# Kernel optimization log

Measured on AMD Instinct MI355X. Metric: run time of the kernel, lower is better.

The kernel has to match this reference:

```python
import jax, jax.numpy as jnp
import numpy as np

NH = 16  # num_heads


def _ln(x, eps=1e-6):
    m = x.mean(-1, keepdims=True)
    v = ((x - m) ** 2).mean(-1, keepdims=True)
    return (x - m) * jax.lax.rsqrt(v + eps)


def _mod(z, sh, sc):
    return z * (1 + sc[:, None, :]) + sh[:, None, :]


def _attn(q, k, v, out_w, out_b, nh=NH):
    B, S, E = q.shape
    hd = E // nh
    q = q.reshape(B, S, nh, hd)
    k = k.reshape(B, -1, nh, hd)
    v = v.reshape(B, -1, nh, hd)
    s = jnp.einsum('bqhd,bkhd->bhqk', q, k) / float(np.sqrt(hd))
    a = jax.nn.softmax(s, axis=-1)
    o = jnp.einsum('bhqk,bkhd->bqhd', a, v).reshape(B, S, E)
    return o @ out_w.T + out_b


def setup_inputs() -> dict:
    key = jax.random.key(0)
    ks = jax.random.split(key, 40)
    E, L, Ne, I, p, C, clip, Kd = 1024, 2, 8, 4096, 2, 4, 768, 1536
    N = (64 // p) ** 2
    n = lambda k, shape, s=0.02: (jax.random.normal(k, shape, jnp.float32) * s)
    inp = {
        'x': jax.random.normal(ks[0], (2, C, 64, 64), jnp.float32),
        't': jax.random.uniform(ks[1], (2,), jnp.float32) * 1000.0,
        'clip_vec': jax.random.normal(ks[2], (2, clip), jnp.float32),
        'qwen_context': jax.random.normal(ks[3], (2, 256, Kd), jnp.float32),
        'conv_w': n(ks[4], (E, C, p, p)),
        'conv_b': n(ks[5], (E,)),
        'pos_embed': n(ks[6], (1, N, E)),
        'tmlp_w1': n(ks[7], (256, 256)), 'tmlp_b1': n(ks[8], (256,)),
        'tmlp_w2': n(ks[9], (256, 256)), 'tmlp_b2': n(ks[10], (256,)),
        'cond_w': n(ks[11], (E, 256 + clip)), 'cond_b': n(ks[12], (E,)),
        'ada_w': n(ks[13], (L, 9 * E, E)), 'ada_b': n(ks[14], (L, 9 * E)),
        'sa_in_w': n(ks[15], (L, 3 * E, E)), 'sa_in_b': n(ks[16], (L, 3 * E)),
        'sa_out_w': n(ks[17], (L, E, E)), 'sa_out_b': n(ks[18], (L, E)),
        'ca_q_w': n(ks[19], (L, E, E)), 'ca_k_w': n(ks[20], (L, E, Kd)),
        'ca_v_w': n(ks[21], (L, E, Kd)), 'ca_in_b': n(ks[22], (L, 3 * E)),
        'ca_out_w': n(ks[23], (L, E, E)), 'ca_out_b': n(ks[24], (L, E)),
        'gate_w': n(ks[25], (L, Ne, E)), 'gate_b': n(ks[26], (L, Ne)),
        'e_w1': n(ks[27], (L, Ne, I, E)), 'e_b1': n(ks[28], (L, Ne, I)),
        'e_w2': n(ks[29], (L, Ne, E, I)), 'e_b2': n(ks[30], (L, Ne, E)),
        'fin_w': n(ks[31], (p * p * C, E)), 'fin_b': n(ks[32], (p * p * C,)),
    }
    return inp


def reference(x, t, clip_vec, qwen_context, conv_w, conv_b, pos_embed,
              tmlp_w1, tmlp_b1, tmlp_w2, tmlp_b2, cond_w, cond_b,
              ada_w, ada_b, sa_in_w, sa_in_b, sa_out_w, sa_out_b,
              ca_q_w, ca_k_w, ca_v_w, ca_in_b, ca_out_w, ca_out_b,
              gate_w, gate_b, e_w1, e_b1, e_w2, e_b2, fin_w, fin_b):
    B, C, H, W = x.shape
    E, p = conv_w.shape[0], conv_w.shape[-1]
    h, w = H // p, W // p
    # patch-embed conv (kernel==stride) as unfold + matmul
    patches = x.reshape(B, C, h, p, w, p).transpose(0, 2, 4, 1, 3, 5).reshape(B, h * w, C * p * p)
    xt = patches @ conv_w.reshape(E, -1).T + conv_b + pos_embed
    # sinusoidal timestep embedding (dim 256)
    half = 128
    freqs = jnp.exp(jnp.arange(half, dtype=jnp.float32) * (-np.log(10000.0) / (half - 1)))
    te = t[:, None] * freqs[None, :]
    te = jnp.concatenate([jnp.sin(te), jnp.cos(te)], -1)
    te = jax.nn.silu(te @ tmlp_w1.T + tmlp_b1) @ tmlp_w2.T + tmlp_b2
    c = jnp.concatenate([te, clip_vec], -1) @ cond_w.T + cond_b  # [B,E]
    depth = ada_w.shape[0]
    for i in range(depth):
        pr = jax.nn.silu(c) @ ada_w[i].T + ada_b[i]
        sh_sa, sc_sa, g_sa, sh_ca, sc_ca, g_ca, sh_m, sc_m, g_m = jnp.split(pr, 9, axis=1)
        # self-attention
        xn = _mod(_ln(xt), sh_sa, sc_sa)
        qkv = xn @ sa_in_w[i].T + sa_in_b[i]
        q, k, v = jnp.split(qkv, 3, axis=-1)
        xt = xt + g_sa[:, None, :] * _attn(q, k, v, sa_out_w[i], sa_out_b[i])
        # cross-attention with separate q/k/v projections
        xn = _mod(_ln(xt), sh_ca, sc_ca)
        q = xn @ ca_q_w[i].T + ca_in_b[i, :E]
        k = qwen_context @ ca_k_w[i].T + ca_in_b[i, E:2 * E]
        v = qwen_context @ ca_v_w[i].T + ca_in_b[i, 2 * E:]
        xt = xt + g_ca[:, None, :] * _attn(q, k, v, ca_out_w[i], ca_out_b[i])
        # top-2 sparse MoE (dense-combine formulation: zero weight for unrouted experts)
        xn = _mod(_ln(xt), sh_m, sc_m)
        probs = jax.nn.softmax(xn @ gate_w[i].T + gate_b[i], axis=-1)
        tw, ti = jax.lax.top_k(probs, 2)
        tw = tw / (tw.sum(-1, keepdims=True) + 1e-6)
        wd = (jax.nn.one_hot(ti, probs.shape[-1], dtype=xn.dtype) * tw[..., None]).sum(-2)  # [B,S,Ne]
        hid = jax.nn.gelu(jnp.einsum('bsd,eid->bsei', xn, e_w1[i]) + e_b1[i], approximate=True)
        y = jnp.einsum('bsei,eoi->bseo', hid, e_w2[i]) + e_b2[i]
        moe = jnp.einsum('bseo,bse->bso', y, wd)
        xt = xt + g_m[:, None, :] * moe
    # final layer + unpatchify (nhwpqc->nchpwq)
    xt = _ln(xt) @ fin_w.T + fin_b
    out = xt.reshape(B, h, w, p, p, C).transpose(0, 5, 1, 3, 2, 4).reshape(B, C, h * p, w * p)
    return out
```

## Files before the change

kernel.cpp:

```cpp
#include <hip/hip_runtime.h>
#include <hip/hip_bf16.h>

#define B_ 2
#define S_ 1024
#define E_ 1024
#define NHEAD 16
#define NE 8
#define II 4096
#define KD 1536
#define CLIP_ 768
#define TOK (B_*S_)
#define NSLOTP 5120

typedef short bf16x8 __attribute__((ext_vector_type(8)));
typedef float f32x4 __attribute__((ext_vector_type(4)));

__device__ __forceinline__ float siluf(float x){ return x/(1.f+expf(-x)); }
__device__ __forceinline__ float geluf(float x){
    float x3 = x*x*x;
    return 0.5f*x*(1.f+tanhf(0.7978845608028654f*(x+0.044715f*x3)));
}
__device__ __forceinline__ unsigned short h16(float x){
    union { __hip_bfloat16 b; unsigned short u; } c;
    c.b = __float2bfloat16(x);
    return c.u;
}
__device__ __forceinline__ unsigned pk2(float a, float b){
    return (unsigned)h16(a) | ((unsigned)h16(b)<<16);
}
__device__ __forceinline__ void sp(float a, unsigned& hb, unsigned& lb){
    unsigned short h = h16(a);
    float r = a - __uint_as_float(((unsigned)h)<<16);
    hb = h; lb = h16(r);
}
__device__ __forceinline__ size_t pidx(int row, int k, int K){
    return (((size_t)(row>>4)*(K>>5) + (k>>5))<<9) + (((k>>3)&3)<<7) + ((row&15)<<3) + (k&7);
}
__device__ __forceinline__ void gload16(const unsigned short* g, unsigned short* l){
    __builtin_amdgcn_global_load_lds((const __attribute__((address_space(1))) void*)g,
                                     (__attribute__((address_space(3))) void*)l, 16, 0, 0);
}

union U8 { unsigned u[4]; bf16x8 v; uint4 q; };

__global__ void k_patch_embed(const float* __restrict__ x, const float* __restrict__ cw,
                              const float* __restrict__ cb, const float* __restrict__ pos,
                              float* __restrict__ xt){
    int token = blockIdx.x;
    int b = token >> 10, n = token & 1023;
    int hh = n >> 5, ww = n & 31;
    __shared__ float patch[16];
    int tid = threadIdx.x;
    if (tid < 16){
        int c = tid >> 2, py = (tid >> 1) & 1, px = tid & 1;
        patch[tid] = x[(((size_t)b*4 + c)*64 + hh*2+py)*64 + ww*2+px];
    }
    __syncthreads();
    for (int e = tid; e < E_; e += 256){
        float acc = cb[e];
        #pragma unroll
        for (int j=0;j<16;j++) acc += patch[j]*cw[e*16+j];
        xt[(size_t)token*E_ + e] = acc + pos[(size_t)n*E_ + e];
    }
}

__global__ void k_time_mlp(const float* __restrict__ t,
                           const float* __restrict__ w1, const float* __restrict__ b1,
                           const float* __restrict__ w2, const float* __restrict__ b2,
                           float* __restrict__ te2g){
    int b = blockIdx.x, tid = threadIdx.x;
    __shared__ float te[256], h1[256];
    if (tid < 128){
        float f = expf((float)tid * (-9.210340371976184f/127.f));
        float a = t[b]*f;
        te[tid]     = sinf(a);
        te[tid+128] = cosf(a);
    }
    __syncthreads();
    {
        float acc = b1[tid];
        const float* wr = w1 + (size_t)tid*256;
        for (int k=0;k<256;k++) acc += te[k]*wr[k];
        h1[tid] = siluf(acc);
    }
    __syncthreads();
    {
        float acc = b2[tid];
        const float* wr = w2 + (size_t)tid*256;
        for (int k=0;k<256;k++) acc += h1[k]*wr[k];
        te2g[b*256+tid] = acc;
    }
}

__global__ void k_cond(const float* __restrict__ te2g, const float* __restrict__ clip,
                       const float* __restrict__ cw, const float* __restrict__ cb,
                       float* __restrict__ silu_c){
    int idx = blockIdx.x*4 + (threadIdx.x>>6);
    int lane = threadIdx.x & 63;
    int b = idx >> 10, e = idx & 1023;
    const float* wr = cw + (size_t)e*1024;
    float acc = 0.f;
    for (int k=lane; k<1024; k+=64){
        float xv = (k<256)? te2g[b*256+k] : clip[b*CLIP_ + k-256];
        acc += xv*wr[k];
    }
    #pragma unroll
    for (int off=32; off; off>>=1) acc += __shfl_down(acc,off);
    if (lane==0) silu_c[b*E_+e] = siluf(acc + cb[e]);
}

__global__ void k_ada2(const float* __restrict__ sic, const float* __restrict__ aw,
                       const float* __restrict__ ab, float* __restrict__ pr){
    int row = blockIdx.x*4 + (threadIdx.x>>6);
    int lane = threadIdx.x & 63;
    const float* w = aw + (size_t)row*1024;
    float a0 = 0.f, a1 = 0.f;
    #pragma unroll
    for (int it=0; it<4; it++){
        int k = it*256 + lane*4;
        float4 wv = *(const float4*)(w+k);
        float4 x0 = *(const float4*)(sic+k);
        float4 x1 = *(const float4*)(sic+1024+k);
        a0 += wv.x*x0.x + wv.y*x0.y + wv.z*x0.z + wv.w*x0.w;
        a1 += wv.x*x1.x + wv.y*x1.y + wv.z*x1.z + wv.w*x1.w;
    }
    #pragma unroll
    for (int off=32; off; off>>=1){ a0 += __shfl_down(a0,off); a1 += __shfl_down(a1,off); }
    if (lane==0){
        float bb = ab[row];
        pr[row] = a0 + bb;
        pr[9*E_ + row] = a1 + bb;
    }
}

template<int PACK>
__global__ void k_ln_mod(const float* __restrict__ src, float* __restrict__ dst32,
                         unsigned short* __restrict__ dsth, unsigned short* __restrict__ dstl,
                         const float* __restrict__ pr, int shc, int scc){
    int token = blockIdx.x, tid = threadIdx.x;
    int b = token >> 10;
    const float* row = src + (size_t)token*E_;
    float4 v = *(const float4*)(row + tid*4);
    float s = v.x+v.y+v.z+v.w;
    float ss = v.x*v.x+v.y*v.y+v.z*v.z+v.w*v.w;
    #pragma unroll
    for (int off=32; off; off>>=1){ s += __shfl_down(s,off); ss += __shfl_down(ss,off); }
    __shared__ float rs_[4], rss_[4];
    int wid = tid >> 6;
    if ((tid&63)==0){ rs_[wid]=s; rss_[wid]=ss; }
    __syncthreads();
    s  = rs_[0]+rs_[1]+rs_[2]+rs_[3];
    ss = rss_[0]+rss_[1]+rss_[2]+rss_[3];
    float mean = s*(1.f/1024.f);
    float rstd = rsqrtf(ss*(1.f/1024.f) - mean*mean + 1e-6f);
    const float* shv = pr + b*9*E_ + shc*E_;
    const float* scv = pr + b*9*E_ + scc*E_;
    int e = tid*4;
    float o[4];
    float4 sc4 = *(const float4*)(scv+e);
    float4 sh4 = *(const float4*)(shv+e);
    o[0] = (v.x-mean)*rstd*(1.f+sc4.x) + sh4.x;
    o[1] = (v.y-mean)*rstd*(1.f+sc4.y) + sh4.y;
    o[2] = (v.z-mean)*rstd*(1.f+sc4.z) + sh4.z;
    o[3] = (v.w-mean)*rstd*(1.f+sc4.w) + sh4.w;
    unsigned hu[2], lu[2];
    {
        unsigned h0,l0,h1,l1;
        sp(o[0],h0,l0); sp(o[1],h1,l1);
        hu[0]=h0|(h1<<16); lu[0]=l0|(l1<<16);
        sp(o[2],h0,l0); sp(o[3],h1,l1);
        hu[1]=h0|(h1<<16); lu[1]=l0|(l1<<16);
    }
    if (PACK){
        size_t base = pidx(token, e, E_);
        *(uint2*)(dsth + base) = make_uint2(hu[0],hu[1]);
        *(uint2*)(dstl + base) = make_uint2(lu[0],lu[1]);
    } else {
        *(float4*)(dst32 + (size_t)token*E_ + e) = make_float4(o[0],o[1],o[2],o[3]);
        *(uint2*)(dsth + (size_t)token*E_ + e) = make_uint2(hu[0],hu[1]);
        *(uint2*)(dstl + (size_t)token*E_ + e) = make_uint2(lu[0],lu[1]);
    }
}

__global__ void k_pack_qwen(const float* __restrict__ q, unsigned short* __restrict__ hp,
                            unsigned short* __restrict__ lp){
    int r = blockIdx.x;
    int k = threadIdx.x*8;
    float f[8];
    *(float4*)(f+0) = *(const float4*)(q + (size_t)r*KD + k);
    *(float4*)(f+4) = *(const float4*)(q + (size_t)r*KD + k + 4);
    U8 H, L;
    #pragma unroll
    for (int i=0;i<4;i++){
        unsigned h0,l0,h1,l1;
        sp(f[2*i],h0,l0); sp(f[2*i+1],h1,l1);
        H.u[i] = h0|(h1<<16); L.u[i] = l0|(l1<<16);
    }
    size_t dst = pidx(r, k, KD);
    *(uint4*)(hp + dst) = H.q;
    *(uint4*)(lp + dst) = L.q;
}

__global__ void k_gather_pack(const unsigned short* __restrict__ xh,
                              const unsigned short* __restrict__ xl,
                              const int* __restrict__ list,
                              unsigned short* __restrict__ oh, unsigned short* __restrict__ ol){
    int s = blockIdx.x;
    int tid = threadIdx.x;
    int token = list[s];
    int k = tid*8;
    size_t src = (size_t)token*E_ + k;
    size_t dst = pidx(s, k, E_);
    *(uint4*)(oh + dst) = *(const uint4*)(xh + src);
    *(uint4*)(ol + dst) = *(const uint4*)(xl + src);
}

template<int NPL>
__global__ void k_pack_w(const float* __restrict__ W, unsigned short* __restrict__ hp,
                         unsigned short* __restrict__ lp, int K){
    int rg = blockIdx.x;
    int t = threadIdx.x;
    int K32 = K>>5;
    for (int k = t*8; k < K; k += 1024){
        size_t bb = (((size_t)rg*K32 + (k>>5))<<9) + (((k>>3)&3)<<7);
        #pragma unroll 4
        for (int r=0;r<16;r++){
            const float* src = W + (size_t)(rg*16 + r)*K + k;
            float f[8];
            *(float4*)(f)   = *(const float4*)src;
            *(float4*)(f+4) = *(const float4*)(src+4);
            U8 H, L;
            #pragma unroll
            for (int i2=0;i2<4;i2++){
                unsigned h0,l0,h1,l1;
                sp(f[2*i2],h0,l0); sp(f[2*i2+1],h1,l1);
                H.u[i2]=h0|(h1<<16); L.u[i2]=l0|(l1<<16);
            }
            *(uint4*)(hp + bb + (r<<3)) = H.q;
            if (NPL==2) *(uint4*)(lp + bb + (r<<3)) = L.q;
        }
    }
}

template<int MOE, int EPI, int TERMS, int SPLITK=1>
__global__ __launch_bounds__(256) void k_mm(
    const unsigned short* __restrict__ Ah, const unsigned short* __restrict__ Al,
    const unsigned short* __restrict__ Bh, const unsigned short* __restrict__ Bl,
    const float* __restrict__ biasp, int bstride,
    void* __restrict__ Cp, void* __restrict__ Cp2, void* __restrict__ Cp3, void* __restrict__ Cp4,
    int ldc, int M, int N, int K,
    const float* __restrict__ pr, int gch,
    const int* __restrict__ cnt, const int* __restrict__ offs)
{
    constexpr int NPL = (TERMS==3)?2:1;
    constexpr int NB  = 2*NPL*8;
    constexpr int NBW = NB/4;
    int e  = MOE ? blockIdx.z : 0;
    int Mm = MOE ? cnt[e] : M;
    int bm = blockIdx.y*128;
    if (MOE && bm >= Mm) return;
    int o0 = MOE ? offs[e] : 0;
    int nt = gridDim.x / SPLITK;
    int ntile = blockIdx.x % nt;
    int kc0 = blockIdx.x / nt;
    int bn = ntile*128;
    int K32 = K >> 5;
    int kbeg = kc0*(K/SPLITK), kend = kbeg + K/SPLITK;
    const float* bias = biasp + (size_t)e*bstride;

    __shared__ __align__(16) unsigned short LDm[2][NB*512];

    int tid = threadIdx.x, lane = tid&63, wid = tid>>6;
    int wm = wid>>1, wn = wid&1;
    int fr = lane&15, fr4 = (lane>>4)*4;
    int l8 = lane<<3;
    int a16 = ((MOE? o0:0) + bm) >> 4;
    int b16 = bn >> 4;
    size_t eoff = (size_t)e * N * K;

    const unsigned short* gb[NBW];
    #pragma unroll
    for (int i=0;i<NBW;i++){
        int bidx = wid*NBW + i;
        int isB = (bidx >= NPL*8) ? 1 : 0;
        int r = bidx - isB*NPL*8;
        int pl = r>>3, rg = r&7;
        const unsigned short* p;
        size_t rgg;
        if (!isB){ p = (TERMS==3 && pl)? Al : Ah; rgg = (size_t)(a16 + rg); }
        else     { p = ((TERMS==3 && pl)? Bl : Bh) + eoff; rgg = (size_t)(b16 + rg); }
        gb[i] = p + ((rgg*K32)<<9) + l8;
    }

    f32x4 acc[4][4];
    #pragma unroll
    for (int m=0;m<4;m++)
        #pragma unroll
        for (int n=0;n<4;n++) acc[m][n] = (f32x4){0.f,0.f,0.f,0.f};

    {
        int kc = kbeg>>5;
        #pragma unroll
        for (int i=0;i<NBW;i++)
            gload16(gb[i] + ((size_t)kc<<9), &LDm[0][(size_t)(wid*NBW+i)<<9]);
    }
    __syncthreads();
    int cur = 0;
    for (int k0=kbeg; k0<kend; k0+=32){
        bool nxt = (k0+32) < kend;
        if (nxt){
            int kc = (k0+32)>>5;
            #pragma unroll
            for (int i=0;i<NBW;i++)
                gload16(gb[i] + ((size_t)kc<<9), &LDm[cur^1][(size_t)(wid*NBW+i)<<9]);
        }
        bf16x8 ah[4], al[4], bh[4], bl[4];
        #pragma unroll
        for (int m=0;m<4;m++){
            ah[m] = *(const bf16x8*)&LDm[cur][(size_t)((wm*4+m)<<9) + l8];
            if (TERMS==3) al[m] = *(const bf16x8*)&LDm[cur][(size_t)((8+wm*4+m)<<9) + l8];
        }
        #pragma unroll
        for (int n=0;n<4;n++){
            bh[n] = *(const bf16x8*)&LDm[cur][(size_t)((NPL*8 + wn*4+n)<<9) + l8];
            if (TERMS==3) bl[n] = *(const bf16x8*)&LDm[cur][(size_t)((NPL*8+8 + wn*4+n)<<9) + l8];
        }
        #pragma unroll
        for (int m=0;m<4;m++)
            #pragma unroll
            for (int n=0;n<4;n++){
                acc[m][n] = __builtin_amdgcn_mfma_f32_16x16x32_bf16(ah[m], bh[n], acc[m][n], 0, 0, 0);
                if (TERMS==3){
                    acc[m][n] = __builtin_amdgcn_mfma_f32_16x16x32_bf16(ah[m], bl[n], acc[m][n], 0, 0, 0);
                    acc[m][n] = __builtin_amdgcn_mfma_f32_16x16x32_bf16(al[m], bh[n], acc[m][n], 0, 0, 0);
                }
            }
        __syncthreads();
        cur ^= 1;
    }

    #pragma unroll
    for (int m=0;m<4;m++){
        #pragma unroll
        for (int j=0;j<4;j++){
            int row = bm + wm*64 + m*16 + fr4 + j;
            if (EPI != 2 && row >= Mm) continue;
            #pragma unroll
            for (int n=0;n<4;n++){
                int col = bn + wn*64 + n*16 + fr;
                float bv = (SPLITK==1 || kc0==0) ? bias[col] : 0.f;
                float v = acc[m][n][j] + bv;
                if (EPI==0){
                    ((float*)Cp)[(size_t)row*ldc + col] = v;
                } else if (EPI==1){
                    int bb = row >> 10;
                    ((float*)Cp)[(size_t)row*ldc + col] += pr[bb*9*E_ + gch*E_ + col] * v;
                } else if (EPI==2){
                    size_t pi = pidx(o0 + row, col, II);
                    if (TERMS==3){
                        unsigned hb, lb; sp(geluf(v), hb, lb);
                        ((unsigned short*)Cp )[pi] = (unsigned short)hb;
                        ((unsigned short*)Cp2)[pi] = (unsigned short)lb;
                    } else {
                        ((unsigned short*)Cp )[pi] = h16(geluf(v));
                    }
                } else if (EPI==3){
                    if (SPLITK==1)
                        ((float*)Cp)[(size_t)(o0+row)*ldc + col] = v;
                    else
                        atomicAdd(&((float*)Cp)[(size_t)(o0+row)*ldc + col], v);
                } else if (EPI==4){
                    if (col < 1024){
                        ((float*)Cp)[(size_t)row*1024 + col] = v;
                    } else {
                        int c2 = col - 1024;
                        int isv = c2 >> 10;
                        int cc = c2 & 1023;
                        int hh2 = cc >> 6, d = cc & 63;
                        size_t idx = (((size_t)(row>>10)*NHEAD + hh2)*1024 + (row & 1023))*64 + d;
                        unsigned hb, lb; sp(v, hb, lb);
                        if (!isv){
                            ((unsigned short*)Cp2)[idx] = (unsigned short)hb;
                            ((unsigned short*)Cp3)[idx] = (unsigned short)lb;
                        } else {
                            ((unsigned*)Cp4)[idx] = hb | (lb<<16);
                        }
                    }
                } else if (EPI==5){
                    int hh2 = col >> 6, d = col & 63;
                    size_t idx = (((size_t)(row>>8)*NHEAD + hh2)*256 + (row & 255))*64 + d;
                    unsigned hb, lb; sp(v, hb, lb);
                    ((unsigned short*)Cp )[idx] = (unsigned short)hb;
                    ((unsigned short*)Cp2)[idx] = (unsigned short)lb;
                } else {
                    int hh2 = col >> 6, d = col & 63;
                    size_t idx = (((size_t)(row>>8)*NHEAD + hh2)*256 + (row & 255))*64 + d;
                    unsigned hb, lb; sp(v, hb, lb);
                    ((unsigned*)Cp)[idx] = hb | (lb<<16);
                }
            }
        }
    }
}

__global__ __launch_bounds__(256) void k_attn_m(
    const float* __restrict__ qp, int qstride,
    const unsigned short* __restrict__ Khp, const unsigned short* __restrict__ Klp,
    const unsigned* __restrict__ Vip,
    unsigned short* __restrict__ oph, unsigned short* __restrict__ opl,
    int Sq, int Sk, float scale)
{
    __shared__ __align__(16) unsigned short Kh[64*72];
    __shared__ __align__(16) unsigned short Kl[64*72];
    __shared__ __align__(16) unsigned V_i[64*70];
    __shared__ __align__(16) unsigned short P_[4][2][16*72];

    int tid = threadIdx.x, lane = tid & 63, wid = tid >> 6;
    int g = lane >> 4, fr = lane & 15;
    int h = blockIdx.y, b = blockIdx.z;
    int qbase = blockIdx.x*64;
    size_t bhbase = (size_t)(b*NHEAD + h)*Sk*64;

    bf16x8 qh[2], ql[2];
    {
        const float* qr = qp + (size_t)(b*Sq + qbase + wid*16 + fr)*qstride + h*64;
        #pragma unroll
        for (int ds=0; ds<2; ds++){
            float f[8];
            *(float4*)(f+0) = *(const float4*)(qr + ds*32 + g*8);
            *(float4*)(f+4) = *(const float4*)(qr + ds*32 + g*8 + 4);
            U8 uh, ul;
            #pragma unroll
            for (int i=0;i<4;i++){
                unsigned h0,l0,h1,l1;
                sp(f[2*i]*scale, h0,l0); sp(f[2*i+1]*scale, h1,l1);
                uh.u[i] = h0|(h1<<16); ul.u[i] = l0|(l1<<16);
            }
            qh[ds] = uh.v; ql[ds] = ul.v;
        }
    }

    float m_run = -1e30f, l_run = 0.f;
    f32x4 oacc[4];
    #pragma unroll
    for (int dt=0;dt<4;dt++) oacc[dt] = (f32x4){0.f,0.f,0.f,0.f};

    unsigned short* PhW = &P_[wid][0][0];
    unsigned short* PlW = &P_[wid][1][0];

    for (int kt0 = 0; kt0 < Sk; kt0 += 64){
        __syncthreads();
        {
            int srow = tid >> 2, d0 = (tid & 3) << 4;
            size_t gidx = bhbase + (size_t)(kt0 + srow)*64 + d0;
            int base = srow*72 + d0;
            *(uint4*)&Kh[base]   = *(const uint4*)(Khp + gidx);
            *(uint4*)&Kh[base+8] = *(const uint4*)(Khp + gidx + 8);
            *(uint4*)&Kl[base]   = *(const uint4*)(Klp + gidx);
            *(uint4*)&Kl[base+8] = *(const uint4*)(Klp + gidx + 8);
            const unsigned* vsrc = Vip + gidx;
            int vb = srow*70 + d0;
            #pragma unroll
            for (int i4=0;i4<4;i4++){
                uint4 u = *(const uint4*)(vsrc + i4*4);
                *(uint2*)&V_i[vb + i4*4]     = make_uint2(u.x,u.y);
                *(uint2*)&V_i[vb + i4*4 + 2] = make_uint2(u.z,u.w);
            }
        }
        __syncthreads();

        f32x4 st[4];
        #pragma unroll
        for (int kt=0;kt<4;kt++) st[kt] = (f32x4){0.f,0.f,0.f,0.f};
        #pragma unroll
        for (int ds=0; ds<2; ds++){
            #pragma unroll
            for (int kt=0;kt<4;kt++){
                int row = kt*16 + fr;
                int so = row*72 + ds*32 + g*8;
                bf16x8 kh  = *(const bf16x8*)&Kh[so];
                bf16x8 klo = *(const bf16x8*)&Kl[so];
                st[kt] = __builtin_amdgcn_mfma_f32_16x16x32_bf16(kh, qh[ds], st[kt], 0,0,0);
                st[kt] = __builtin_amdgcn_mfma_f32_16x16x32_bf16(kh, ql[ds], st[kt], 0,0,0);
                st[kt] = __builtin_amdgcn_mfma_f32_16x16x32_bf16(klo, qh[ds], st[kt], 0,0,0);
            }
        }

        float pmax = -1e30f;
        #pragma unroll
        for (int kt=0;kt<4;kt++)
            #pragma unroll
            for (int r=0;r<4;r++) pmax = fmaxf(pmax, st[kt][r]);
        pmax = fmaxf(pmax, __shfl_xor(pmax, 16));
        pmax = fmaxf(pmax, __shfl_xor(pmax, 32));
        float mnew = fmaxf(m_run, pmax);
        float p[4][4]; float psum = 0.f;
        #pragma unroll
        for (int kt=0;kt<4;kt++)
            #pragma unroll
            for (int r=0;r<4;r++){ float pv = expf(st[kt][r] - mnew); p[kt][r] = pv; psum += pv; }
        psum += __shfl_xor(psum, 16);
        psum += __shfl_xor(psum, 32);
        float corr = expf(m_run - mnew);
        l_run = l_run*corr + psum;
        m_run = mnew;
        #pragma unroll
        for (int j=0;j<4;j++){
            float cj = __shfl(corr, g*4 + j);
            #pragma unroll
            for (int dt=0;dt<4;dt++) oacc[dt][j] *= cj;
        }

        #pragma unroll
        for (int kt=0;kt<4;kt++){
            unsigned h0,l0,h1,l1,h2,l2,h3,l3;
            sp(p[kt][0],h0,l0); sp(p[kt][1],h1,l1);
            sp(p[kt][2],h2,l2); sp(p[kt][3],h3,l3);
            int base = fr*72 + kt*16 + g*4;
            *(unsigned*)&PhW[base]     = h0|(h1<<16);
            *(unsigned*)&PhW[base + 2] = h2|(h3<<16);
            *(unsigned*)&PlW[base]     = l0|(l1<<16);
            *(unsigned*)&PlW[base + 2] = l2|(l3<<16);
        }

        #pragma unroll
        for (int ks=0; ks<2; ks++){
            int pso = fr*72 + ks*32 + g*8;
            bf16x8 ph = *(const bf16x8*)&PhW[pso];
            bf16x8 pl = *(const bf16x8*)&PlW[pso];
            #pragma unroll
            for (int dt=0; dt<4; dt++){
                unsigned w[8];
                #pragma unroll
                for (int j=0;j<8;j++){
                    int row = ks*32 + g*8 + j;
                    w[j] = V_i[row*70 + dt*16 + fr];
                }
                U8 vh, vl;
                #pragma unroll
                for (int i=0;i<4;i++){
                    vh.u[i] = (w[2*i] & 0xffffu) | (w[2*i+1] << 16);
                    vl.u[i] = (w[2*i] >> 16)     | (w[2*i+1] & 0xffff0000u);
                }
                oacc[dt] = __builtin_amdgcn_mfma_f32_16x16x32_bf16(ph, vh.v, oacc[dt], 0,0,0);
                oacc[dt] = __builtin_amdgcn_mfma_f32_16x16x32_bf16(ph, vl.v, oacc[dt], 0,0,0);
                oacc[dt] = __builtin_amdgcn_mfma_f32_16x16x32_bf16(pl, vh.v, oacc[dt], 0,0,0);
            }
        }
    }

    float linv = 1.f / l_run;
    #pragma unroll
    for (int j=0;j<4;j++){
        float lj = __shfl(linv, g*4 + j);
        int row = b*Sq + qbase + wid*16 + g*4 + j;
        #pragma unroll
        for (int dt=0;dt<4;dt++){
            unsigned hb, lb; sp(oacc[dt][j]*lj, hb, lb);
            int k = h*64 + dt*16 + fr;
            size_t pi = pidx(row, k, E_);
            oph[pi] = (unsigned short)hb;
            opl[pi] = (unsigned short)lb;
        }
    }
}

__global__ void k_route(const float* __restrict__ xn, const float* __restrict__ gw,
                        const float* __restrict__ gb, int* __restrict__ i01,
                        float* __restrict__ w01, int* __restrict__ cnt){
    int token = blockIdx.x, lane = threadIdx.x;
    const float* row = xn + (size_t)token*E_;
    float part[8] = {0,0,0,0,0,0,0,0};
    for (int k = lane; k < E_; k += 64){
        float xv = row[k];
        #pragma unroll
        for (int e=0;e<8;e++) part[e] += xv*gw[e*E_+k];
    }
    #pragma unroll
    for (int e=0;e<8;e++){
        #pragma unroll
        for (int off=32; off; off>>=1) part[e] += __shfl_down(part[e], off);
    }
    if (lane==0){
        float lg[8]; float mx = -1e30f;
        #pragma unroll
        for (int e=0;e<8;e++){ lg[e] = part[e]+gb[e]; if (lg[e]>mx) mx = lg[e]; }
        float sum = 0.f;
        #pragma unroll
        for (int e=0;e<8;e++){ lg[e] = expf(lg[e]-mx); sum += lg[e]; }
        int a0 = 0;
        #pragma unroll
        for (int e=1;e<8;e++) if (lg[e] > lg[a0]) a0 = e;
        int a1 = (a0==0)?1:0;
        #pragma unroll
        for (int e=0;e<8;e++) if (e!=a0 && lg[e] > lg[a1]) a1 = e;
        float p0 = lg[a0]/sum, p1 = lg[a1]/sum;
        float inv = 1.f/(p0+p1+1e-6f);
        i01[token*2+0]=a0; i01[token*2+1]=a1;
        w01[token*2+0]=p0*inv; w01[token*2+1]=p1*inv;
        atomicAdd(&cnt[a0],1); atomicAdd(&cnt[a1],1);
    }
}

__global__ void k_scan(const int* __restrict__ cnt, int* __restrict__ offs, int* __restrict__ curs){
    if (threadIdx.x==0 && blockIdx.x==0){
        int o = 0;
        for (int e=0;e<8;e++){
            offs[e]=o; curs[e]=o;
            o += ((cnt[e]+127)>>7)<<7;
        }
    }
}

__global__ void k_place(const int* __restrict__ i01,
                        int* __restrict__ curs, int* __restrict__ list,
                        int* __restrict__ t2s){
    int t = blockIdx.x*256 + threadIdx.x;
    if (t >= TOK) return;
    #pragma unroll
    for (int s=0;s<2;s++){
        int e = i01[t*2+s];
        int p = atomicAdd(&curs[e],1);
        list[p] = t;
        t2s[t*2+s] = p;
    }
}

__global__ void k_moe_combine2(float* __restrict__ xt, const float* __restrict__ yslot,
                               const int* __restrict__ t2s, const float* __restrict__ w01,
                               const float* __restrict__ pr){
    int idx = blockIdx.x*256 + threadIdx.x;
    int token = idx >> 10, n = idx & 1023;
    int b = token >> 10;
    int s0 = t2s[token*2], s1 = t2s[token*2+1];
    float mo = w01[token*2]*yslot[(size_t)s0*E_+n] + w01[token*2+1]*yslot[(size_t)s1*E_+n];
    xt[idx] += pr[b*9*E_ + 8*E_ + n]*mo;
}

__global__ void k_final(const float* __restrict__ xt, const float* __restrict__ fw,
                        const float* __restrict__ fb, float* __restrict__ out){
    int token = blockIdx.x, tid = threadIdx.x;
    int b = token >> 10, n = token & 1023, hh = n >> 5, ww = n & 31;
    const float* row = xt + (size_t)token*E_;
    float4 v = *(const float4*)(row + tid*4);
    float s = v.x+v.y+v.z+v.w;
    float ss = v.x*v.x+v.y*v.y+v.z*v.z+v.w*v.w;
    #pragma unroll
    for (int off=32; off; off>>=1){ s += __shfl_down(s,off); ss += __shfl_down(ss,off); }
    __shared__ float rs_[4], rss_[4];
    int wid = tid >> 6;
    if ((tid&63)==0){ rs_[wid]=s; rss_[wid]=ss; }
    __syncthreads();
    s  = rs_[0]+rs_[1]+rs_[2]+rs_[3];
    ss = rss_[0]+rss_[1]+rss_[2]+rss_[3];
    float mean = s*(1.f/1024.f);
    float rstd = rsqrtf(ss*(1.f/1024.f) - mean*mean + 1e-6f);
    __shared__ float xl[1024];
    int e = tid*4;
    xl[e+0]=(v.x-mean)*rstd; xl[e+1]=(v.y-mean)*rstd;
    xl[e+2]=(v.z-mean)*rstd; xl[e+3]=(v.w-mean)*rstd;
    __syncthreads();
    int o = tid & 15, seg = tid >> 4;
    float part = 0.f;
    const float* wr = fw + (size_t)o*E_ + seg*64;
    const float* xr = xl + seg*64;
    #pragma unroll 8
    for (int j=0;j<64;j++) part += xr[j]*wr[j];
    __shared__ float ps[16][17];
    ps[seg][o] = part;
    __syncthreads();
    if (tid < 16){
        float acc = fb[tid];
        #pragma unroll
        for (int s2=0;s2<16;s2++) acc += ps[s2][tid];
        int py = tid>>3, px = (tid>>2)&1, ch = tid&3;
        out[(((size_t)b*4+ch)*64 + hh*2+py)*64 + ww*2+px] = acc;
    }
}

extern "C" void kernel_launch(void* const* d_in, const int* in_sizes, int n_in,
                              void* d_out, int out_size, void* d_ws, size_t ws_size,
                              hipStream_t stream){
    const float* x        = (const float*)d_in[0];
    const float* t        = (const float*)d_in[1];
    const float* clip     = (const float*)d_in[2];
    const float* qwen     = (const float*)d_in[3];
    const float* conv_w   = (const float*)d_in[4];
    const float* conv_b   = (const float*)d_in[5];
    const float* pos      = (const float*)d_in[6];
    const float* tw1      = (const float*)d_in[7];
    const float* tb1      = (const float*)d_in[8];
    const float* tw2      = (const float*)d_in[9];
    const float* tb2      = (const float*)d_in[10];
    const float* cond_w   = (const float*)d_in[11];
    const float* cond_b   = (const float*)d_in[12];
    const float* ada_w    = (const float*)d_in[13];
    const float* ada_b    = (const float*)d_in[14];
    const float* sa_in_w  = (const float*)d_in[15];
    const float* sa_in_b  = (const float*)d_in[16];
    const float* sa_out_w = (const float*)d_in[17];
    const float* sa_out_b = (const float*)d_in[18];
    const float* ca_q_w   = (const float*)d_in[19];
    const float* ca_k_w   = (const float*)d_in[20];
    const float* ca_v_w   = (const float*)d_in[21];
    const float* ca_in_b  = (const float*)d_in[22];
    const float* ca_out_w = (const float*)d_in[23];
    const float* ca_out_b = (const float*)d_in[24];
    const float* gate_w   = (const float*)d_in[25];
    const float* gate_b   = (const float*)d_in[26];
    const float* e_w1     = (const float*)d_in[27];
    const float* e_b1     = (const float*)d_in[28];
    const float* e_w2     = (const float*)d_in[29];
    const float* e_b2     = (const float*)d_in[30];
    const float* fin_w    = (const float*)d_in[31];
    const float* fin_b    = (const float*)d_in[32];

    float* ws    = (float*)d_ws;
    float* xt    = ws;
    float* xn    = ws + 2097152;
    float* qbuf  = ws + 4194304;
    unsigned short* Khp = (unsigned short*)(ws + 6291456);
    unsigned short* Klp = (unsigned short*)(ws + 7340032);
    unsigned*       Vip = (unsigned*)(ws + 8388608);
    float* yslot = ws + 4194304;
    unsigned short* xnh  = (unsigned short*)(ws + 10485760);
    unsigned short* xnl  = (unsigned short*)(ws + 11534336);
    unsigned short* obh  = (unsigned short*)(ws + 12582912);
    unsigned short* obl  = (unsigned short*)(ws + 13631488);
    unsigned short* xnsh = (unsigned short*)(ws + 14680064);
    unsigned short* xnsl = (unsigned short*)(ws + 17301504);
    unsigned short* hidh = (unsigned short*)(ws + 19922944);
    unsigned short* hidl = (unsigned short*)(ws + 30408704);
    unsigned short* qwph = (unsigned short*)(ws + 40894464);
    unsigned short* qwpl = (unsigned short*)(ws + 41287680);
    float* pr    = ws + 42729472;
    float* sic   = ws + 42747904;
    float* w01   = ws + 42749952;
    int*   i01   = (int*)(ws + 42754048);
    int*   t2s   = (int*)(ws + 42758144);
    int*   list  = (int*)(ws + 42762240);
    int*   cnt   = (int*)(ws + 42767360);
    int*   offs  = cnt + 8;
    int*   curs  = cnt + 16;
    float* te2g  = ws + 42767872;
    unsigned short* wb = (unsigned short*)(ws + 42768384);

    const size_t SA_IN_H=0, SA_IN_L=3145728, SA_OUT_H=6291456, SA_OUT_L=7340032;
    const size_t CAQ_H=8388608, CAQ_L=9437184, CAK_H=10485760, CAK_L=12058624;
    const size_t CAV_H=13631488, CAV_L=15204352, CAO_H=16777216, CAO_L=17825792;
    const size_t W_H=0, W_L=16777216;

    k_patch_embed<<<TOK,256,0,stream>>>(x, conv_w, conv_b, pos, xt);
    k_time_mlp<<<B_,256,0,stream>>>(t, tw1, tb1, tw2, tb2, te2g);
    k_cond<<<512,256,0,stream>>>(te2g, clip, cond_w, cond_b, sic);
    k_pack_qwen<<<B_*256,192,0,stream>>>(qwen, qwph, qwpl);

    for (int i=0;i<2;i++){
        k_ada2<<<2304,256,0,stream>>>(sic, ada_w + (size_t)i*9*E_*E_,
                                      ada_b + (size_t)i*9*E_, pr);
        k_pack_w<2><<<192,128,0,stream>>>(sa_in_w + (size_t)i*3*E_*E_, wb+SA_IN_H, wb+SA_IN_L, E_);
        k_pack_w<2><<<64,128,0,stream>>>(sa_out_w + (size_t)i*E_*E_, wb+SA_OUT_H, wb+SA_OUT_L, E_);
        k_pack_w<2><<<64,128,0,stream>>>(ca_q_w + (size_t)i*E_*E_, wb+CAQ_H, wb+CAQ_L, E_);
        k_pack_w<2><<<64,128,0,stream>>>(ca_k_w + (size_t)i*E_*KD, wb+CAK_H, wb+CAK_L, KD);
        k_pack_w<2><<<64,128,0,stream>>>(ca_v_w + (size_t)i*E_*KD, wb+CAV_H, wb+CAV_L, KD);
        k_pack_w<2><<<64,128,0,stream>>>(ca_out_w + (size_t)i*E_*E_, wb+CAO_H, wb+CAO_L, E_);
        k_ln_mod<1><<<TOK,256,0,stream>>>(xt, nullptr, xnh, xnl, pr, 0, 1);
        k_mm<0,4,3><<<dim3(24,16),256,0,stream>>>(
            xnh, xnl, wb+SA_IN_H, wb+SA_IN_L, sa_in_b + (size_t)i*3*E_, 0,
            qbuf, Khp, Klp, Vip, 0, TOK, 3*E_, E_, nullptr, 0, nullptr, nullptr);
        k_attn_m<<<dim3(16,NHEAD,B_),256,0,stream>>>(qbuf, E_, Khp, Klp, Vip,
                                                     obh, obl, S_, S_, 0.125f);
        k_mm<0,1,3><<<dim3(8,16),256,0,stream>>>(
            obh, obl, wb+SA_OUT_H, wb+SA_OUT_L, sa_out_b + (size_t)i*E_, 0,
            xt, nullptr, nullptr, nullptr, E_, TOK, E_, E_, pr, 2, nullptr, nullptr);
        k_ln_mod<1><<<TOK,256,0,stream>>>(xt, nullptr, xnh, xnl, pr, 3, 4);
        k_mm<0,0,3><<<dim3(8,16),256,0,stream>>>(
            xnh, xnl, wb+CAQ_H, wb+CAQ_L, ca_in_b + (size_t)i*3*E_, 0,
            qbuf, nullptr, nullptr, nullptr, E_, TOK, E_, E_, nullptr, 0, nullptr, nullptr);
        k_mm<0,5,3><<<dim3(8,4),256,0,stream>>>(
            qwph, qwpl, wb+CAK_H, wb+CAK_L, ca_in_b + (size_t)i*3*E_ + E_, 0,
            Khp, Klp, nullptr, nullptr, 0, B_*256, E_, KD, nullptr, 0, nullptr, nullptr);
        k_mm<0,6,3><<<dim3(8,4),256,0,stream>>>(
            qwph, qwpl, wb+CAV_H, wb+CAV_L, ca_in_b + (size_t)i*3*E_ + 2*E_, 0,
            Vip, nullptr, nullptr, nullptr, 0, B_*256, E_, KD, nullptr, 0, nullptr, nullptr);
        k_attn_m<<<dim3(16,NHEAD,B_),256,0,stream>>>(qbuf, E_, Khp, Klp, Vip,
                                                     obh, obl, S_, 256, 0.125f);
        k_mm<0,1,3><<<dim3(8,16),256,0,stream>>>(
            obh, obl, wb+CAO_H, wb+CAO_L, ca_out_b + (size_t)i*E_, 0,
            xt, nullptr, nullptr, nullptr, E_, TOK, E_, E_, pr, 5, nullptr, nullptr);
        k_ln_mod<0><<<TOK,256,0,stream>>>(xt, xn, xnh, xnl, pr, 6, 7);
        hipMemsetAsync(cnt, 0, 8*sizeof(int), stream);
        hipMemsetAsync(list, 0, NSLOTP*sizeof(int), stream);
        k_route<<<TOK,64,0,stream>>>(xn, gate_w + (size_t)i*NE*E_, gate_b + (size_t)i*NE,
                                     i01, w01, cnt);
        k_scan<<<1,64,0,stream>>>(cnt, offs, curs);
        k_place<<<TOK/256,256,0,stream>>>(i01, curs, list, t2s);
        k_gather_pack<<<NSLOTP,128,0,stream>>>(xnh, xnl, list, xnsh, xnsl);
        hipMemsetAsync(yslot, 0, (size_t)NSLOTP*E_*sizeof(float), stream);
        if (i==0){
            for (int e0=0;e0<NE;e0+=4){
                k_pack_w<2><<<1024,128,0,stream>>>(e_w1 + ((size_t)i*NE+e0)*II*E_, wb+W_H, wb+W_L, E_);
                k_mm<1,2,3><<<dim3(32,32,4),256,0,stream>>>(
                    xnsh, xnsl, wb+W_H, wb+W_L, e_b1 + (size_t)i*NE*II + (size_t)e0*II, II,
                    hidh, hidl, nullptr, nullptr, II, 0, II, E_, nullptr, 0, cnt+e0, offs+e0);
            }
            for (int e0=0;e0<NE;e0+=4){
                k_pack_w<2><<<256,128,0,stream>>>(e_w2 + ((size_t)i*NE+e0)*E_*II, wb+W_H, wb+W_L, II);
                k_mm<1,3,3,4><<<dim3(32,32,4),256,0,stream>>>(
                    hidh, hidl, wb+W_H, wb+W_L, e_b2 + (size_t)i*NE*E_ + (size_t)e0*E_, E_,
                    yslot, nullptr, nullptr, nullptr, E_, 0, E_, II, nullptr, 0, cnt+e0, offs+e0);
            }
        } else {
            k_pack_w<1><<<2048,128,0,stream>>>(e_w1 + (size_t)i*NE*II*E_, wb+W_H, nullptr, E_);
            k_mm<1,2,1><<<dim3(32,32,NE),256,0,stream>>>(
                xnsh, nullptr, wb+W_H, nullptr, e_b1 + (size_t)i*NE*II, II,
                hidh, nullptr, nullptr, nullptr, II, 0, II, E_, nullptr, 0, cnt, offs);
            k_pack_w<1><<<512,128,0,stream>>>(e_w2 + (size_t)i*NE*E_*II, wb+W_H, nullptr, II);
            k_mm<1,3,1,4><<<dim3(32,32,NE),256,0,stream>>>(
                hidh, nullptr, wb+W_H, nullptr, e_b2 + (size_t)i*NE*E_, E_,
                yslot, nullptr, nullptr, nullptr, E_, 0, E_, II, nullptr, 0, cnt, offs);
        }
        k_moe_combine2<<<TOK*E_/256,256,0,stream>>>(xt, yslot, t2s, w01, pr);
    }
    k_final<<<TOK,256,0,stream>>>(xt, fin_w, fin_b, (float*)d_out);
}
```

Measured before the change: 2.319 ms.

## Fuse weight bf16 split/pack into GEMM B-tile staging, drop pack kernels

Removes the separate k_pack_w passes that converted fp32 weights into blocked hi/lo bf16 buffers. The GEMM now loads fp32 weight rows directly into registers, splits them into hi/lo bf16 and writes them to shared memory inside the main loop, with the next tile's global load issued before the MFMAs. This saves a full write and re-read of the packed weights per layer and allows all 8 experts to run in one launch. In exchange, every M-tile block re-reads and re-converts the fp32 weights (twice the bytes of bf16), and the B staging now adds register pressure and ALU work to the inner loop.

Result: no change. 2.298 ms (-0.9%).

```diff
diff --git a/kernel.cpp b/kernel.cpp
--- a/kernel.cpp
+++ b/kernel.cpp
@@ -24,9 +24,6 @@
     union { __hip_bfloat16 b; unsigned short u; } c;
     c.b = __float2bfloat16(x);
     return c.u;
-}
-__device__ __forceinline__ unsigned pk2(float a, float b){
-    return (unsigned)h16(a) | ((unsigned)h16(b)<<16);
 }
 __device__ __forceinline__ void sp(float a, unsigned& hb, unsigned& lb){
     unsigned short h = h16(a);
@@ -215,37 +212,10 @@
     *(uint4*)(ol + dst) = *(const uint4*)(xl + src);
 }
 
-template<int NPL>
-__global__ void k_pack_w(const float* __restrict__ W, unsigned short* __restrict__ hp,
-                         unsigned short* __restrict__ lp, int K){
-    int rg = blockIdx.x;
-    int t = threadIdx.x;
-    int K32 = K>>5;
-    for (int k = t*8; k < K; k += 1024){
-        size_t bb = (((size_t)rg*K32 + (k>>5))<<9) + (((k>>3)&3)<<7);
-        #pragma unroll 4
-        for (int r=0;r<16;r++){
-            const float* src = W + (size_t)(rg*16 + r)*K + k;
-            float f[8];
-            *(float4*)(f)   = *(const float4*)src;
-            *(float4*)(f+4) = *(const float4*)(src+4);
-            U8 H, L;
-            #pragma unroll
-            for (int i2=0;i2<4;i2++){
-                unsigned h0,l0,h1,l1;
-                sp(f[2*i2],h0,l0); sp(f[2*i2+1],h1,l1);
-                H.u[i2]=h0|(h1<<16); L.u[i2]=l0|(l1<<16);
-            }
-            *(uint4*)(hp + bb + (r<<3)) = H.q;
-            if (NPL==2) *(uint4*)(lp + bb + (r<<3)) = L.q;
-        }
-    }
-}
-
 template<int MOE, int EPI, int TERMS, int SPLITK=1>
 __global__ __launch_bounds__(256) void k_mm(
     const unsigned short* __restrict__ Ah, const unsigned short* __restrict__ Al,
-    const unsigned short* __restrict__ Bh, const unsigned short* __restrict__ Bl,
+    const float* __restrict__ Wp, int ldw,
     const float* __restrict__ biasp, int bstride,
     void* __restrict__ Cp, void* __restrict__ Cp2, void* __restrict__ Cp3, void* __restrict__ Cp4,
     int ldc, int M, int N, int K,
@@ -253,8 +223,8 @@
     const int* __restrict__ cnt, const int* __restrict__ offs)
 {
     constexpr int NPL = (TERMS==3)?2:1;
-    constexpr int NB  = 2*NPL*8;
-    constexpr int NBW = NB/4;
+    constexpr int NAB = NPL*8;
+    constexpr int NABW = NAB/4;
     int e  = MOE ? blockIdx.z : 0;
     int Mm = MOE ? cnt[e] : M;
     int bm = blockIdx.y*128;
@@ -268,29 +238,51 @@
     int kbeg = kc0*(K/SPLITK), kend = kbeg + K/SPLITK;
     const float* bias = biasp + (size_t)e*bstride;
 
-    __shared__ __align__(16) unsigned short LDm[2][NB*512];
+    __shared__ __align__(16) unsigned short A_[2][NAB*512];
+    __shared__ __align__(16) unsigned short Bs_[2][NAB*512];
 
     int tid = threadIdx.x, lane = tid&63, wid = tid>>6;
     int wm = wid>>1, wn = wid&1;
     int fr = lane&15, fr4 = (lane>>4)*4;
     int l8 = lane<<3;
     int a16 = ((MOE? o0:0) + bm) >> 4;
-    int b16 = bn >> 4;
-    size_t eoff = (size_t)e * N * K;
-
-    const unsigned short* gb[NBW];
-    #pragma unroll
-    for (int i=0;i<NBW;i++){
-        int bidx = wid*NBW + i;
-        int isB = (bidx >= NPL*8) ? 1 : 0;
-        int r = bidx - isB*NPL*8;
-        int pl = r>>3, rg = r&7;
-        const unsigned short* p;
-        size_t rgg;
-        if (!isB){ p = (TERMS==3 && pl)? Al : Ah; rgg = (size_t)(a16 + rg); }
-        else     { p = ((TERMS==3 && pl)? Bl : Bh) + eoff; rgg = (size_t)(b16 + rg); }
-        gb[i] = p + ((rgg*K32)<<9) + l8;
-    }
+
+    const unsigned short* ga[NABW];
+    #pragma unroll
+    for (int i=0;i<NABW;i++){
+        int blk = wid*NABW + i;
+        int pl = blk>>3, rg = blk&7;
+        const unsigned short* p = (TERMS==3 && pl)? Al : Ah;
+        ga[i] = p + (((size_t)(a16+rg)*K32)<<9) + l8;
+    }
+
+    int srow = tid >> 1, shalf = tid & 1;
+    const float* Bf = Wp + (size_t)e*N*ldw + (size_t)(bn + srow)*ldw + shalf*16;
+    int brg = srow >> 4, brr = srow & 15;
+    int bbase0 = brg*512 + (shalf*2)*128 + brr*8;
+
+    float fB[16];
+    auto LOADB = [&](int k0){
+        *(float4*)(fB+0)  = *(const float4*)(Bf+k0+0);
+        *(float4*)(fB+4)  = *(const float4*)(Bf+k0+4);
+        *(float4*)(fB+8)  = *(const float4*)(Bf+k0+8);
+        *(float4*)(fB+12) = *(const float4*)(Bf+k0+12);
+    };
+    auto STAGEB = [&](int buf){
+        unsigned hb2[8], lb2[8];
+        #pragma unroll
+        for (int i=0;i<8;i++){
+            unsigned h0,l0,h1,l1;
+            sp(fB[2*i],h0,l0); sp(fB[2*i+1],h1,l1);
+            hb2[i]=h0|(h1<<16); lb2[i]=l0|(l1<<16);
+        }
+        *(uint4*)&Bs_[buf][bbase0]       = make_uint4(hb2[0],hb2[1],hb2[2],hb2[3]);
+        *(uint4*)&Bs_[buf][bbase0 + 128] = make_uint4(hb2[4],hb2[5],hb2[6],hb2[7]);
+        if (TERMS==3){
+            *(uint4*)&Bs_[buf][4096 + bbase0]       = make_uint4(lb2[0],lb2[1],lb2[2],lb2[3]);
+            *(uint4*)&Bs_[buf][4096 + bbase0 + 128] = make_uint4(lb2[4],lb2[5],lb2[6],lb2[7]);
+        }
+    };
 
     f32x4 acc[4][4];
     #pragma unroll
@@ -301,9 +293,11 @@
     {
         int kc = kbeg>>5;
         #pragma unroll
-        for (int i=0;i<NBW;i++)
-            gload16(gb[i] + ((size_t)kc<<9), &LDm[0][(size_t)(wid*NBW+i)<<9]);
-    }
+        for (int i=0;i<NABW;i++)
+            gload16(ga[i] + ((size_t)kc<<9), &A_[0][(size_t)(wid*NABW+i)<<9]);
+    }
+    LOADB(kbeg);
+    STAGEB(0);
     __syncthreads();
     int cur = 0;
     for (int k0=kbeg; k0<kend; k0+=32){
@@ -311,19 +305,20 @@
         if (nxt){
             int kc = (k0+32)>>5;
             #pragma unroll
-            for (int i=0;i<NBW;i++)
-                gload16(gb[i] + ((size_t)kc<<9), &LDm[cur^1][(size_t)(wid*NBW+i)<<9]);
+            for (int i=0;i<NABW;i++)
+                gload16(ga[i] + ((size_t)kc<<9), &A_[cur^1][(size_t)(wid*NABW+i)<<9]);
+            LOADB(k0+32);
         }
         bf16x8 ah[4], al[4], bh[4], bl[4];
         #pragma unroll
         for (int m=0;m<4;m++){
-            ah[m] = *(const bf16x8*)&LDm[cur][(size_t)((wm*4+m)<<9) + l8];
-            if (TERMS==3) al[m] = *(const bf16x8*)&LDm[cur][(size_t)((8+wm*4+m)<<9) + l8];
+            ah[m] = *(const bf16x8*)&A_[cur][(wm*4+m)*512 + l8];
+            if (TERMS==3) al[m] = *(const bf16x8*)&A_[cur][(8+wm*4+m)*512 + l8];
         }
         #pragma unroll
         for (int n=0;n<4;n++){
-            bh[n] = *(const bf16x8*)&LDm[cur][(size_t)((NPL*8 + wn*4+n)<<9) + l8];
-            if (TERMS==3) bl[n] = *(const bf16x8*)&LDm[cur][(size_t)((NPL*8+8 + wn*4+n)<<9) + l8];
+            bh[n] = *(const bf16x8*)&Bs_[cur][(wn*4+n)*512 + l8];
+            if (TERMS==3) bl[n] = *(const bf16x8*)&Bs_[cur][(8+wn*4+n)*512 + l8];
         }
         #pragma unroll
         for (int m=0;m<4;m++)
@@ -335,6 +330,7 @@
                     acc[m][n] = __builtin_amdgcn_mfma_f32_16x16x32_bf16(al[m], bh[n], acc[m][n], 0, 0, 0);
                 }
             }
+        if (nxt) STAGEB(cur^1);
         __syncthreads();
         cur ^= 1;
     }
@@ -743,12 +739,6 @@
     int*   offs  = cnt + 8;
     int*   curs  = cnt + 16;
     float* te2g  = ws + 42767872;
-    unsigned short* wb = (unsigned short*)(ws + 42768384);
-
-    const size_t SA_IN_H=0, SA_IN_L=3145728, SA_OUT_H=6291456, SA_OUT_L=7340032;
-    const size_t CAQ_H=8388608, CAQ_L=9437184, CAK_H=10485760, CAK_L=12058624;
-    const size_t CAV_H=13631488, CAV_L=15204352, CAO_H=16777216, CAO_L=17825792;
-    const size_t W_H=0, W_L=16777216;
 
     k_patch_embed<<<TOK,256,0,stream>>>(x, conv_w, conv_b, pos, xt);
     k_time_mlp<<<B_,256,0,stream>>>(t, tw1, tb1, tw2, tb2, te2g);
@@ -758,35 +748,29 @@
     for (int i=0;i<2;i++){
         k_ada2<<<2304,256,0,stream>>>(sic, ada_w + (size_t)i*9*E_*E_,
                                       ada_b + (size_t)i*9*E_, pr);
-        k_pack_w<2><<<192,128,0,stream>>>(sa_in_w + (size_t)i*3*E_*E_, wb+SA_IN_H, wb+SA_IN_L, E_);
-        k_pack_w<2><<<64,128,0,stream>>>(sa_out_w + (size_t)i*E_*E_, wb+SA_OUT_H, wb+SA_OUT_L, E_);
-        k_pack_w<2><<<64,128,0,stream>>>(ca_q_w + (size_t)i*E_*E_, wb+CAQ_H, wb+CAQ_L, E_);
-        k_pack_w<2><<<64,128,0,stream>>>(ca_k_w + (size_t)i*E_*KD, wb+CAK_H, wb+CAK_L, KD);
-        k_pack_w<2><<<64,128,0,stream>>>(ca_v_w + (size_t)i*E_*KD, wb+CAV_H, wb+CAV_L, KD);
-        k_pack_w<2><<<64,128,0,stream>>>(ca_out_w + (size_t)i*E_*E_, wb+CAO_H, wb+CAO_L, E_);
         k_ln_mod<1><<<TOK,256,0,stream>>>(xt, nullptr, xnh, xnl, pr, 0, 1);
         k_mm<0,4,3><<<dim3(24,16),256,0,stream>>>(
-            xnh, xnl, wb+SA_IN_H, wb+SA_IN_L, sa_in_b + (size_t)i*3*E_, 0,
+            xnh, xnl, sa_in_w + (size_t)i*3*E_*E_, E_, sa_in_b + (size_t)i*3*E_, 0,
             qbuf, Khp, Klp, Vip, 0, TOK, 3*E_, E_, nullptr, 0, nullptr, nullptr);
         k_attn_m<<<dim3(16,NHEAD,B_),256,0,stream>>>(qbuf, E_, Khp, Klp, Vip,
                                                      obh, obl, S_, S_, 0.125f);
         k_mm<0,1,3><<<dim3(8,16),256,0,stream>>>(
-            obh, obl, wb+SA_OUT_H, wb+SA_OUT_L, sa_out_b + (size_t)i*E_, 0,
+            obh, obl, sa_out_w + (size_t)i*E_*E_, E_, sa_out_b + (size_t)i*E_, 0,
             xt, nullptr, nullptr, nullptr, E_, TOK, E_, E_, pr, 2, nullptr, nullptr);
         k_ln_mod<1><<<TOK,256,0,stream>>>(xt, nullptr, xnh, xnl, pr, 3, 4);
         k_mm<0,0,3><<<dim3(8,16),256,0,stream>>>(
-            xnh, xnl, wb+CAQ_H, wb+CAQ_L, ca_in_b + (size_t)i*3*E_, 0,
+            xnh, xnl, ca_q_w + (size_t)i*E_*E_, E_, ca_in_b + (size_t)i*3*E_, 0,
             qbuf, nullptr, nullptr, nullptr, E_, TOK, E_, E_, nullptr, 0, nullptr, nullptr);
         k_mm<0,5,3><<<dim3(8,4),256,0,stream>>>(
-            qwph, qwpl, wb+CAK_H, wb+CAK_L, ca_in_b + (size_t)i*3*E_ + E_, 0,
+            qwph, qwpl, ca_k_w + (size_t)i*E_*KD, KD, ca_in_b + (size_t)i*3*E_ + E_, 0,
             Khp, Klp, nullptr, nullptr, 0, B_*256, E_, KD, nullptr, 0, nullptr, nullptr);
         k_mm<0,6,3><<<dim3(8,4),256,0,stream>>>(
-            qwph, qwpl, wb+CAV_H, wb+CAV_L, ca_in_b + (size_t)i*3*E_ + 2*E_, 0,
+            qwph, qwpl, ca_v_w + (size_t)i*E_*KD, KD, ca_in_b + (size_t)i*3*E_ + 2*E_, 0,
             Vip, nullptr, nullptr, nullptr, 0, B_*256, E_, KD, nullptr, 0, nullptr, nullptr);
         k_attn_m<<<dim3(16,NHEAD,B_),256,0,stream>>>(qbuf, E_, Khp, Klp, Vip,
                                                      obh, obl, S_, 256, 0.125f);
         k_mm<0,1,3><<<dim3(8,16),256,0,stream>>>(
-            obh, obl, wb+CAO_H, wb+CAO_L, ca_out_b + (size_t)i*E_, 0,
+            obh, obl, ca_out_w + (size_t)i*E_*E_, E_, ca_out_b + (size_t)i*E_, 0,
             xt, nullptr, nullptr, nullptr, E_, TOK, E_, E_, pr, 5, nullptr, nullptr);
         k_ln_mod<0><<<TOK,256,0,stream>>>(xt, xn, xnh, xnl, pr, 6, 7);
         hipMemsetAsync(cnt, 0, 8*sizeof(int), stream);
@@ -798,26 +782,18 @@
         k_gather_pack<<<NSLOTP,128,0,stream>>>(xnh, xnl, list, xnsh, xnsl);
         hipMemsetAsync(yslot, 0, (size_t)NSLOTP*E_*sizeof(float), stream);
         if (i==0){
-            for (int e0=0;e0<NE;e0+=4){
-                k_pack_w<2><<<1024,128,0,stream>>>(e_w1 + ((size_t)i*NE+e0)*II*E_, wb+W_H, wb+W_L, E_);
-                k_mm<1,2,3><<<dim3(32,32,4),256,0,stream>>>(
-                    xnsh, xnsl, wb+W_H, wb+W_L, e_b1 + (size_t)i*NE*II + (size_t)e0*II, II,
-                    hidh, hidl, nullptr, nullptr, II, 0, II, E_, nullptr, 0, cnt+e0, offs+e0);
-            }
-            for (int e0=0;e0<NE;e0+=4){
-                k_pack_w<2><<<256,128,0,stream>>>(e_w2 + ((size_t)i*NE+e0)*E_*II, wb+W_H, wb+W_L, II);
-                k_mm<1,3,3,4><<<dim3(32,32,4),256,0,stream>>>(
-                    hidh, hidl, wb+W_H, wb+W_L, e_b2 + (size_t)i*NE*E_ + (size_t)e0*E_, E_,
-                    yslot, nullptr, nullptr, nullptr, E_, 0, E_, II, nullptr, 0, cnt+e0, offs+e0);
-            }
+            k_mm<1,2,3><<<dim3(32,32,NE),256,0,stream>>>(
+                xnsh, xnsl, e_w1 + (size_t)i*NE*II*E_, E_, e_b1 + (size_t)i*NE*II, II,
+                hidh, hidl, nullptr, nullptr, II, 0, II, E_, nullptr, 0, cnt, offs);
+            k_mm<1,3,3,4><<<dim3(32,32,NE),256,0,stream>>>(
+                hidh, hidl, e_w2 + (size_t)i*NE*E_*II, II, e_b2 + (size_t)i*NE*E_, E_,
+                yslot, nullptr, nullptr, nullptr, E_, 0, E_, II, nullptr, 0, cnt, offs);
         } else {
-            k_pack_w<1><<<2048,128,0,stream>>>(e_w1 + (size_t)i*NE*II*E_, wb+W_H, nullptr, E_);
             k_mm<1,2,1><<<dim3(32,32,NE),256,0,stream>>>(
-                xnsh, nullptr, wb+W_H, nullptr, e_b1 + (size_t)i*NE*II, II,
+                xnsh, nullptr, e_w1 + (size_t)i*NE*II*E_, E_, e_b1 + (size_t)i*NE*II, II,
                 hidh, nullptr, nullptr, nullptr, II, 0, II, E_, nullptr, 0, cnt, offs);
-            k_pack_w<1><<<512,128,0,stream>>>(e_w2 + (size_t)i*NE*E_*II, wb+W_H, nullptr, II);
             k_mm<1,3,1,4><<<dim3(32,32,NE),256,0,stream>>>(
-                hidh, nullptr, wb+W_H, nullptr, e_b2 + (size_t)i*NE*E_, E_,
+                hidh, nullptr, e_w2 + (size_t)i*NE*E_*II, II, e_b2 + (size_t)i*NE*E_, E_,
                 yslot, nullptr, nullptr, nullptr, E_, 0, E_, II, nullptr, 0, cnt, offs);
         }
         k_moe_combine2<<<TOK*E_/256,256,0,stream>>>(xt, yslot, t2s, w01, pr);
```
